# Kernel tuning notes

Hardware: AMD Instinct MI355X
Metric: run time of the kernel (lower is better)

The kernel has to match this reference:

```python
import jax, jax.numpy as jnp
import numpy as np

N = 20000
D = 256      # input_dim
F = 256      # output_dim
K = F // 8   # hypernetwork rank (c=8 in source)


def setup_inputs() -> dict:
    key = jax.random.key(0)
    k1, k2, k3, k4, k5 = jax.random.split(key, 5)
    h = jax.random.normal(k1, (N, D), dtype=jnp.float32)
    adj = jax.random.uniform(k2, (N, N), dtype=jnp.float32)
    # xavier-uniform-like small init for params
    W1 = jax.random.normal(k3, (D, K), dtype=jnp.float32) * 0.05
    W2 = jax.random.normal(k4, (K, D, F), dtype=jnp.float32) * 0.05
    b = jax.random.normal(k5, (K, F), dtype=jnp.float32) * 0.05
    return {"h": h, "adj": adj, "W1": W1, "W2": W2, "b": b}


def reference(h, adj, W1, W2, b):
    # node: per-node code vector [N, K]
    node = h @ W1
    # Original: w = einsum('nd,dcf->ncf', node, W2); x = einsum('nc,ncf->nf', h, w)
    # Algebraically identical but avoids the huge [N, D, F] intermediate by
    # contracting the input-dim axis first: [N,K,F] instead of [N,D,F].
    hw = jnp.einsum('nc,kcf->nkf', h, W2)      # [N, K, F]
    x = jnp.einsum('nk,nkf->nf', node, hw)     # [N, F]
    # graph aggregation
    x = adj @ x                                 # [N, F]
    # per-node bias generated from the node code
    x = x + node @ b                            # [N, F]
    return jax.nn.relu(x)
```

## Files before the change

### kernel.cpp

```cpp
#include <hip/hip_runtime.h>
#include <hip/hip_bf16.h>

#define Nn 20000
#define Npad 20160
#define Dd 256
#define Ff 256
#define Kc 32

typedef __attribute__((ext_vector_type(8))) short short8;
typedef __attribute__((ext_vector_type(4))) short short4_t;
typedef __attribute__((ext_vector_type(4))) float float4_t;
typedef __attribute__((ext_vector_type(2))) unsigned int uint2_t;

static __device__ __forceinline__ short f2bf(float x) {
    union { float f; unsigned u; } v; v.f = x;
    unsigned r = v.u + 0x7FFFu + ((v.u >> 16) & 1u);
    return (short)(r >> 16);
}
static __device__ __forceinline__ short4_t cvt4(float4_t v) {
    short4_t r; r[0] = f2bf(v[0]); r[1] = f2bf(v[1]); r[2] = f2bf(v[2]); r[3] = f2bf(v[3]);
    return r;
}
static __device__ __forceinline__ unsigned cvtpk(float a, float b) {
    unsigned r;
    asm("v_cvt_pk_bf16_f32 %0, %1, %2" : "=v"(r) : "v"(a), "v"(b));
    return r;
}

__global__ __launch_bounds__(256) void k_node(const float* __restrict__ h,
                                              const float* __restrict__ W1,
                                              float* __restrict__ node) {
    int t = blockIdx.x * 256 + threadIdx.x;
    int n = t >> 5, k = t & 31;
    if (n >= Nn) return;
    const float4_t* hr = (const float4_t*)(h + (size_t)n * Dd);
    float s = 0.f;
    #pragma unroll 8
    for (int d4 = 0; d4 < 64; ++d4) {
        float4_t hv = hr[d4];
        #pragma unroll
        for (int j = 0; j < 4; ++j) s += hv[j] * W1[(d4 * 4 + j) * Kc + k];
    }
    node[n * Kc + k] = s;
}

__global__ __launch_bounds__(256) void k_packW2(const float* __restrict__ W2,
                                                short* __restrict__ P) {
    int t = blockIdx.x * 256 + threadIdx.x;
    int lane = t & 63;
    int cf = (t >> 6) & 15;
    int dc = (t >> 10) & 7;
    int kk = t >> 13;
    int col = cf * 16 + (lane & 15);
    int d0  = dc * 32 + (lane >> 4) * 8;
    const float* src = W2 + ((size_t)(kk * Dd + d0)) * Ff + col;
    short8 v;
    #pragma unroll
    for (int j = 0; j < 8; ++j) v[j] = f2bf(src[(size_t)j * Ff]);
    *(short8*)(P + (size_t)t * 8) = v;
}

__global__ __launch_bounds__(256, 2) void k_xpre(const float* __restrict__ h,
                                                 const float* __restrict__ node,
                                                 const short* __restrict__ P,
                                                 short* __restrict__ xpre_t) {
    __shared__ short hlds[64 * 264];
    __shared__ float ntl[32 * 64];
    int t = threadIdx.x;
    int n0 = blockIdx.x * 64;

    #pragma unroll
    for (int i = 0; i < 16; ++i) {
        int c = t + i * 256;
        int row = c >> 6, cc = c & 63;
        int n = n0 + row; if (n > Nn - 1) n = Nn - 1;
        float4_t v = *(const float4_t*)(h + (size_t)n * Dd + cc * 4);
        *(short4_t*)&hlds[row * 264 + cc * 4] = cvt4(v);
    }
    #pragma unroll
    for (int i = 0; i < 8; ++i) {
        int idx = t + i * 256;
        int nl = idx >> 5, k = idx & 31;
        int n = n0 + nl; if (n > Nn - 1) n = Nn - 1;
        ntl[k * 64 + nl] = node[(size_t)n * Kc + k];
    }
    __syncthreads();

    int lane = t & 63, w = t >> 6;
    int arow = lane & 15;
    int asel = (lane >> 4) * 8;
    float4_t acc[4][4];
    #pragma unroll
    for (int a = 0; a < 4; ++a)
        #pragma unroll
        for (int b2 = 0; b2 < 4; ++b2) acc[a][b2] = (float4_t){0.f, 0.f, 0.f, 0.f};

    for (int kk = 0; kk < 32; ++kk) {
        float4_t T[4][4];
        #pragma unroll
        for (int a = 0; a < 4; ++a)
            #pragma unroll
            for (int b2 = 0; b2 < 4; ++b2) T[a][b2] = (float4_t){0.f, 0.f, 0.f, 0.f};
        #pragma unroll
        for (int dc = 0; dc < 8; ++dc) {
            short8 af[4], bfr[4];
            #pragma unroll
            for (int rf = 0; rf < 4; ++rf)
                af[rf] = *(const short8*)&hlds[(rf * 16 + arow) * 264 + dc * 32 + asel];
            #pragma unroll
            for (int cf = 0; cf < 4; ++cf)
                bfr[cf] = *(const short8*)(P + ((size_t)(((kk * 8 + dc) * 16 + w * 4 + cf) * 64 + lane)) * 8);
            #pragma unroll
            for (int rf = 0; rf < 4; ++rf)
                #pragma unroll
                for (int cf = 0; cf < 4; ++cf)
                    T[rf][cf] = __builtin_amdgcn_mfma_f32_16x16x32_bf16(af[rf], bfr[cf], T[rf][cf], 0, 0, 0);
        }
        #pragma unroll
        for (int rf = 0; rf < 4; ++rf) {
            float4_t sc = *(const float4_t*)&ntl[kk * 64 + rf * 16 + (lane >> 4) * 4];
            #pragma unroll
            for (int cf = 0; cf < 4; ++cf)
                #pragma unroll
                for (int r = 0; r < 4; ++r)
                    acc[rf][cf][r] += sc[r] * T[rf][cf][r];
        }
    }

    #pragma unroll
    for (int rf = 0; rf < 4; ++rf) {
        int nl = rf * 16 + (lane >> 4) * 4;
        #pragma unroll
        for (int cf = 0; cf < 4; ++cf) {
            int f = w * 64 + cf * 16 + (lane & 15);
            #pragma unroll
            for (int r = 0; r < 4; ++r) {
                int n = n0 + nl + r;
                if (n < Nn)       xpre_t[(size_t)f * Npad + n] = f2bf(acc[rf][cf][r]);
                else if (n < Npad) xpre_t[(size_t)f * Npad + n] = 0;
            }
        }
    }
}

#define BM 80
#define BK 320
#define DCN 10
#define ASTR 328
#define NSTEP 63
#define ALIM (Nn * Nn - 4)

__global__ __launch_bounds__(512, 2) void k_aggr(const float* __restrict__ adj,
                                                 const short* __restrict__ xpre_t,
                                                 const float* __restrict__ node,
                                                 const float* __restrict__ bb,
                                                 float* __restrict__ out) {
    __shared__ short alds[2][BM * ASTR];
    __shared__ float nlds[BM * 32];
    __shared__ float blds[32 * 256];

    const int t = threadIdx.x;
    const int m0 = blockIdx.x * BM;
    const int lane = t & 63, w = t >> 6;
    const int kb = (lane >> 4) * 8;

    #pragma unroll
    for (int i = 0; i < 5; ++i) { int idx = t + i * 512; nlds[idx] = node[(size_t)m0 * 32 + idx]; }
    #pragma unroll
    for (int i = 0; i < 4; ++i) { int idx = t + i * 512; *(float4_t*)&blds[idx * 4] = *(const float4_t*)(bb + (size_t)idx * 4); }

    const bool v13 = (t < 256);
    int gbase[13], loff[13];
    #pragma unroll
    for (int i = 0; i < 13; ++i) {
        int c = t + i * 512; if (c >= 6400) c = 0;
        int row = c / 80, col = c % 80;
        gbase[i] = (m0 + row) * Nn + col * 4;
        loff[i]  = row * ASTR + col * 4;
    }
    const short* xrow0 = xpre_t + (long)(w * 32 + (lane & 15)) * Npad + kb;
    const short* xrow1 = xrow0 + 16L * Npad;

    float4_t acc[5][2];
    #pragma unroll
    for (int rf = 0; rf < 5; ++rf)
        #pragma unroll
        for (int cf = 0; cf < 2; ++cf) acc[rf][cf] = (float4_t){0.f, 0.f, 0.f, 0.f};

    float4_t A[13];
    short8 b0[DCN], b1[DCN];

#define LOADA(s_) do { _Pragma("unroll") for (int i = 0; i < 13; ++i) \
        if (i < 12 || v13) { int idx = gbase[i] + (s_) * BK; \
            if (idx > ALIM) idx = ALIM; \
            A[i] = *(const float4_t*)(adj + idx); } } while (0)

#define WRITEA(buf_) do { _Pragma("unroll") for (int i = 0; i < 13; ++i) \
        if (i < 12 || v13) { \
            uint2_t u = { cvtpk(A[i][0], A[i][1]), cvtpk(A[i][2], A[i][3]) }; \
            *(uint2_t*)&alds[buf_][loff[i]] = u; } } while (0)

#define SYNC() do { asm volatile("s_waitcnt lgkmcnt(0)" ::: "memory"); \
                    __builtin_amdgcn_s_barrier(); } while (0)

    LOADA(0);
    WRITEA(0);
    SYNC();

    #pragma unroll 1
    for (int s = 0; s < NSTEP; ++s) {
        const short* xr0 = xrow0 + (long)s * BK;
        const short* xr1 = xrow1 + (long)s * BK;
        #pragma unroll
        for (int dc = 0; dc < DCN; ++dc) {
            b0[dc] = *(const short8*)(xr0 + dc * 32);
            b1[dc] = *(const short8*)(xr1 + dc * 32);
        }
        if (s + 1 < NSTEP) LOADA(s + 1);

        const short* ar = alds[s & 1];
        #pragma unroll
        for (int dc = 0; dc < DCN; ++dc) {
            #pragma unroll
            for (int rf = 0; rf < 5; ++rf) {
                short8 afr = *(const short8*)&ar[(rf * 16 + (lane & 15)) * ASTR + dc * 32 + kb];
                acc[rf][0] = __builtin_amdgcn_mfma_f32_16x16x32_bf16(afr, b0[dc], acc[rf][0], 0, 0, 0);
                acc[rf][1] = __builtin_amdgcn_mfma_f32_16x16x32_bf16(afr, b1[dc], acc[rf][1], 0, 0, 0);
            }
        }
        if (s + 1 < NSTEP) WRITEA((s & 1) ^ 1);
        SYNC();
    }

    #pragma unroll
    for (int rf = 0; rf < 5; ++rf) {
        #pragma unroll
        for (int cf = 0; cf < 2; ++cf) {
            int fl = w * 32 + cf * 16 + (lane & 15);
            #pragma unroll
            for (int r = 0; r < 4; ++r) {
                int nl = rf * 16 + (lane >> 4) * 4 + r;
                float bias = 0.f;
                #pragma unroll 8
                for (int k = 0; k < 32; ++k) bias += nlds[nl * 32 + k] * blds[k * 256 + fl];
                float v = acc[rf][cf][r] + bias;
                out[(size_t)(m0 + nl) * 256 + fl] = v > 0.f ? v : 0.f;
            }
        }
    }
#undef LOADA
#undef WRITEA
#undef SYNC
}

extern "C" void kernel_launch(void* const* d_in, const int* in_sizes, int n_in,
                              void* d_out, int out_size, void* d_ws, size_t ws_size,
                              hipStream_t stream) {
    const float* h   = (const float*)d_in[0];
    const float* adj = (const float*)d_in[1];
    const float* W1  = (const float*)d_in[2];
    const float* W2  = (const float*)d_in[3];
    const float* b   = (const float*)d_in[4];
    float* out = (float*)d_out;

    char* ws = (char*)d_ws;
    float* node   = (float*)ws;
    short* P      = (short*)(ws + 2560000);
    short* xpre_t = (short*)(ws + 2560000 + 4194304);

    k_node  <<<2500, 256, 0, stream>>>(h, W1, node);
    k_packW2<<<1024, 256, 0, stream>>>(W2, P);
    k_xpre  <<<315,  256, 0, stream>>>(h, node, P, xpre_t);
    k_aggr  <<<250,  512, 0, stream>>>(adj, xpre_t, node, b, out);
}
```

Measured before the change: 924.8 us.

## Restructure aggregation GEMM with direct global-to-LDS adj loads and split bias kernel

Rewrites the adj@x aggregation kernel to use 64-row tiles with a 64-wide K step. The fp32 adj tiles are streamed into a swizzled, double-buffered LDS buffer through global_load_lds, and the bf16 conversion happens at fragment read time. This removes the register staging of A and the separate LDS write pass, and raises occupancy to 4 blocks per CU. The per-node bias is moved into its own kernel that writes the output first, and the aggregation kernel adds it back with a read-modify-write. The trade-offs are many more barrier-separated steps and extra output traffic.

```diff
diff --git a/kernel.cpp b/kernel.cpp
--- a/kernel.cpp
+++ b/kernel.cpp
@@ -2,15 +2,17 @@
 #include <hip/hip_bf16.h>
 
 #define Nn 20000
-#define Npad 20160
 #define Dd 256
 #define Ff 256
 #define Kc 32
 
+#define BK2 64
+#define NSTEP2 313
+#define NP2 20032
+
 typedef __attribute__((ext_vector_type(8))) short short8;
 typedef __attribute__((ext_vector_type(4))) short short4_t;
 typedef __attribute__((ext_vector_type(4))) float float4_t;
-typedef __attribute__((ext_vector_type(2))) unsigned int uint2_t;
 
 static __device__ __forceinline__ short f2bf(float x) {
     union { float f; unsigned u; } v; v.f = x;
@@ -25,6 +27,12 @@
     unsigned r;
     asm("v_cvt_pk_bf16_f32 %0, %1, %2" : "=v"(r) : "v"(a), "v"(b));
     return r;
+}
+static __device__ __forceinline__ void glds16(const float* g, float* l) {
+    __builtin_amdgcn_global_load_lds(
+        (const __attribute__((address_space(1))) unsigned int*)g,
+        (__attribute__((address_space(3))) unsigned int*)l,
+        16, 0, 0);
 }
 
 __global__ __launch_bounds__(256) void k_node(const float* __restrict__ h,
@@ -44,6 +52,17 @@
     node[n * Kc + k] = s;
 }
 
+__global__ __launch_bounds__(256) void k_bias(const float* __restrict__ node,
+                                              const float* __restrict__ bb,
+                                              float* __restrict__ out) {
+    int n = blockIdx.x, f = threadIdx.x;
+    const float* nr = node + (size_t)n * Kc;
+    float s = 0.f;
+    #pragma unroll
+    for (int k = 0; k < Kc; ++k) s += nr[k] * bb[k * Ff + f];
+    out[(size_t)n * Ff + f] = s;
+}
+
 __global__ __launch_bounds__(256) void k_packW2(const float* __restrict__ W2,
                                                 short* __restrict__ P) {
     int t = blockIdx.x * 256 + threadIdx.x;
@@ -136,121 +155,114 @@
             #pragma unroll
             for (int r = 0; r < 4; ++r) {
                 int n = n0 + nl + r;
-                if (n < Nn)       xpre_t[(size_t)f * Npad + n] = f2bf(acc[rf][cf][r]);
-                else if (n < Npad) xpre_t[(size_t)f * Npad + n] = 0;
-            }
-        }
-    }
-}
-
-#define BM 80
-#define BK 320
-#define DCN 10
-#define ASTR 328
-#define NSTEP 63
-#define ALIM (Nn * Nn - 4)
-
-__global__ __launch_bounds__(512, 2) void k_aggr(const float* __restrict__ adj,
+                if (n < Nn)      xpre_t[(size_t)f * NP2 + n] = f2bf(acc[rf][cf][r]);
+                else if (n < NP2) xpre_t[(size_t)f * NP2 + n] = 0;
+            }
+        }
+    }
+}
+
+__global__ __launch_bounds__(512, 4) void k_aggr(const float* __restrict__ adj,
                                                  const short* __restrict__ xpre_t,
-                                                 const float* __restrict__ node,
-                                                 const float* __restrict__ bb,
                                                  float* __restrict__ out) {
-    __shared__ short alds[2][BM * ASTR];
-    __shared__ float nlds[BM * 32];
-    __shared__ float blds[32 * 256];
+    __shared__ float alds[2][4096];
 
     const int t = threadIdx.x;
-    const int m0 = blockIdx.x * BM;
     const int lane = t & 63, w = t >> 6;
-    const int kb = (lane >> 4) * 8;
-
-    #pragma unroll
-    for (int i = 0; i < 5; ++i) { int idx = t + i * 512; nlds[idx] = node[(size_t)m0 * 32 + idx]; }
-    #pragma unroll
-    for (int i = 0; i < 4; ++i) { int idx = t + i * 512; *(float4_t*)&blds[idx * 4] = *(const float4_t*)(bb + (size_t)idx * 4); }
-
-    const bool v13 = (t < 256);
-    int gbase[13], loff[13];
-    #pragma unroll
-    for (int i = 0; i < 13; ++i) {
-        int c = t + i * 512; if (c >= 6400) c = 0;
-        int row = c / 80, col = c % 80;
-        gbase[i] = (m0 + row) * Nn + col * 4;
-        loff[i]  = row * ASTR + col * 4;
-    }
-    const short* xrow0 = xpre_t + (long)(w * 32 + (lane & 15)) * Npad + kb;
-    const short* xrow1 = xrow0 + 16L * Npad;
-
-    float4_t acc[5][2];
-    #pragma unroll
-    for (int rf = 0; rf < 5; ++rf)
-        #pragma unroll
-        for (int cf = 0; cf < 2; ++cf) acc[rf][cf] = (float4_t){0.f, 0.f, 0.f, 0.f};
-
-    float4_t A[13];
-    short8 b0[DCN], b1[DCN];
-
-#define LOADA(s_) do { _Pragma("unroll") for (int i = 0; i < 13; ++i) \
-        if (i < 12 || v13) { int idx = gbase[i] + (s_) * BK; \
-            if (idx > ALIM) idx = ALIM; \
-            A[i] = *(const float4_t*)(adj + idx); } } while (0)
-
-#define WRITEA(buf_) do { _Pragma("unroll") for (int i = 0; i < 13; ++i) \
-        if (i < 12 || v13) { \
-            uint2_t u = { cvtpk(A[i][0], A[i][1]), cvtpk(A[i][2], A[i][3]) }; \
-            *(uint2_t*)&alds[buf_][loff[i]] = u; } } while (0)
-
-#define SYNC() do { asm volatile("s_waitcnt lgkmcnt(0)" ::: "memory"); \
-                    __builtin_amdgcn_s_barrier(); } while (0)
-
-    LOADA(0);
-    WRITEA(0);
-    SYNC();
+    const int wm = w >> 2, wn = w & 3;
+    const int m0 = blockIdx.x * 64;
+
+    long rowbase[2]; int colp[2];
+    #pragma unroll
+    for (int i = 0; i < 2; ++i) {
+        int d = (w * 2 + i) * 256 + lane * 4;
+        int row = d >> 6, col = d & 63;
+        int r = m0 + row; if (r > Nn - 1) r = Nn - 1;
+        rowbase[i] = (long)r * Nn;
+        colp[i] = col ^ ((row & 7) << 2);
+    }
+    const short* bp0 = xpre_t + (long)(wn * 64 +  0 + (lane & 15)) * NP2 + (lane >> 4) * 8;
+    const short* bp1 = xpre_t + (long)(wn * 64 + 16 + (lane & 15)) * NP2 + (lane >> 4) * 8;
+    const short* bp2 = xpre_t + (long)(wn * 64 + 32 + (lane & 15)) * NP2 + (lane >> 4) * 8;
+    const short* bp3 = xpre_t + (long)(wn * 64 + 48 + (lane & 15)) * NP2 + (lane >> 4) * 8;
+
+    float4_t acc[2][4];
+    #pragma unroll
+    for (int rf = 0; rf < 2; ++rf)
+        #pragma unroll
+        for (int cf = 0; cf < 4; ++cf) acc[rf][cf] = (float4_t){0.f, 0.f, 0.f, 0.f};
+
+    short8 Bf[2][4];
+
+    #pragma unroll
+    for (int i = 0; i < 2; ++i)
+        glds16(adj + rowbase[i] + colp[i], &alds[0][(w * 2 + i) * 256]);
 
     #pragma unroll 1
-    for (int s = 0; s < NSTEP; ++s) {
-        const short* xr0 = xrow0 + (long)s * BK;
-        const short* xr1 = xrow1 + (long)s * BK;
-        #pragma unroll
-        for (int dc = 0; dc < DCN; ++dc) {
-            b0[dc] = *(const short8*)(xr0 + dc * 32);
-            b1[dc] = *(const short8*)(xr1 + dc * 32);
-        }
-        if (s + 1 < NSTEP) LOADA(s + 1);
-
-        const short* ar = alds[s & 1];
-        #pragma unroll
-        for (int dc = 0; dc < DCN; ++dc) {
-            #pragma unroll
-            for (int rf = 0; rf < 5; ++rf) {
-                short8 afr = *(const short8*)&ar[(rf * 16 + (lane & 15)) * ASTR + dc * 32 + kb];
-                acc[rf][0] = __builtin_amdgcn_mfma_f32_16x16x32_bf16(afr, b0[dc], acc[rf][0], 0, 0, 0);
-                acc[rf][1] = __builtin_amdgcn_mfma_f32_16x16x32_bf16(afr, b1[dc], acc[rf][1], 0, 0, 0);
-            }
-        }
-        if (s + 1 < NSTEP) WRITEA((s & 1) ^ 1);
-        SYNC();
-    }
-
-    #pragma unroll
-    for (int rf = 0; rf < 5; ++rf) {
-        #pragma unroll
-        for (int cf = 0; cf < 2; ++cf) {
-            int fl = w * 32 + cf * 16 + (lane & 15);
-            #pragma unroll
-            for (int r = 0; r < 4; ++r) {
-                int nl = rf * 16 + (lane >> 4) * 4 + r;
-                float bias = 0.f;
-                #pragma unroll 8
-                for (int k = 0; k < 32; ++k) bias += nlds[nl * 32 + k] * blds[k * 256 + fl];
-                float v = acc[rf][cf][r] + bias;
-                out[(size_t)(m0 + nl) * 256 + fl] = v > 0.f ? v : 0.f;
-            }
-        }
-    }
-#undef LOADA
-#undef WRITEA
-#undef SYNC
+    for (int s = 0; s < NSTEP2; ++s) {
+        const int cur = s & 1;
+        const long so = (long)s * BK2;
+        #pragma unroll
+        for (int dc = 0; dc < 2; ++dc) {
+            Bf[dc][0] = *(const short8*)(bp0 + so + dc * 32);
+            Bf[dc][1] = *(const short8*)(bp1 + so + dc * 32);
+            Bf[dc][2] = *(const short8*)(bp2 + so + dc * 32);
+            Bf[dc][3] = *(const short8*)(bp3 + so + dc * 32);
+        }
+        __builtin_amdgcn_sched_barrier(0);
+        if (s + 1 < NSTEP2) {
+            #pragma unroll
+            for (int i = 0; i < 2; ++i) {
+                int c = (s + 1) * BK2 + colp[i];
+                if (c > Nn - 4) c = Nn - 4;
+                glds16(adj + rowbase[i] + c, &alds[cur ^ 1][(w * 2 + i) * 256]);
+            }
+            __builtin_amdgcn_sched_barrier(0);
+            asm volatile("s_waitcnt vmcnt(2)" ::: "memory");
+        } else {
+            __builtin_amdgcn_sched_barrier(0);
+            asm volatile("s_waitcnt vmcnt(0)" ::: "memory");
+        }
+        __builtin_amdgcn_s_barrier();
+        __builtin_amdgcn_sched_barrier(0);
+
+        const float* ab = alds[cur];
+        #pragma unroll
+        for (int dc = 0; dc < 2; ++dc) {
+            #pragma unroll
+            for (int rf = 0; rf < 2; ++rf) {
+                const int rl = wm * 32 + rf * 16 + (lane & 15);
+                const int sw = (rl & 7) << 2;
+                const int c0 = dc * 32 + (lane >> 4) * 8;
+                float4_t lo = *(const float4_t*)&ab[rl * 64 + ((c0    ) ^ sw)];
+                float4_t hi = *(const float4_t*)&ab[rl * 64 + ((c0 + 4) ^ sw)];
+                union { short8 s8; unsigned u[4]; } af;
+                af.u[0] = cvtpk(lo[0], lo[1]); af.u[1] = cvtpk(lo[2], lo[3]);
+                af.u[2] = cvtpk(hi[0], hi[1]); af.u[3] = cvtpk(hi[2], hi[3]);
+                #pragma unroll
+                for (int cf = 0; cf < 4; ++cf)
+                    acc[rf][cf] = __builtin_amdgcn_mfma_f32_16x16x32_bf16(af.s8, Bf[dc][cf], acc[rf][cf], 0, 0, 0);
+            }
+        }
+        __builtin_amdgcn_s_barrier();
+    }
+
+    #pragma unroll
+    for (int rf = 0; rf < 2; ++rf) {
+        #pragma unroll
+        for (int cf = 0; cf < 4; ++cf) {
+            const int fl = wn * 64 + cf * 16 + (lane & 15);
+            #pragma unroll
+            for (int q = 0; q < 4; ++q) {
+                int n = m0 + wm * 32 + rf * 16 + (lane >> 4) * 4 + q;
+                if (n < Nn) {
+                    float* op = out + (size_t)n * Ff + fl;
+                    float v = acc[rf][cf][q] + *op;
+                    *op = v > 0.f ? v : 0.f;
+                }
+            }
+        }
+    }
 }
 
 extern "C" void kernel_launch(void* const* d_in, const int* in_sizes, int n_in,
@@ -268,8 +280,9 @@
     short* P      = (short*)(ws + 2560000);
     short* xpre_t = (short*)(ws + 2560000 + 4194304);
 
-    k_node  <<<2500, 256, 0, stream>>>(h, W1, node);
-    k_packW2<<<1024, 256, 0, stream>>>(W2, P);
-    k_xpre  <<<315,  256, 0, stream>>>(h, node, P, xpre_t);
-    k_aggr  <<<250,  512, 0, stream>>>(adj, xpre_t, node, b, out);
-}
+    k_node  <<<2500,  256, 0, stream>>>(h, W1, node);
+    k_bias  <<<Nn,    256, 0, stream>>>(node, b, out);
+    k_packW2<<<1024,  256, 0, stream>>>(W2, P);
+    k_xpre  <<<313,   256, 0, stream>>>(h, node, P, xpre_t);
+    k_aggr  <<<313,   512, 0, stream>>>(adj, xpre_t, out);
+}
```

Result: slower. 1.749 ms (+89.2%).
